# Kernel tuning notes

Measured on AMD Instinct MI355X. Metric: run time of the kernel, lower is better.

## Reference

```python
import jax, jax.numpy as jnp
import numpy as np

NUM_HEADS = 8
DIM_HEAD = 64
GROUPS = 32
EPS = 1e-5


def setup_inputs() -> dict:
    key = jax.random.key(0)
    k1, k2, k3 = jax.random.split(key, 3)
    C = 512
    inner = NUM_HEADS * DIM_HEAD  # 512
    x = jax.random.normal(k1, (8, C, 32, 32), dtype=jnp.float32)
    gamma = jnp.ones((C,), dtype=jnp.float32)
    beta = jnp.zeros((C,), dtype=jnp.float32)
    w_qkv = jax.random.normal(k2, (3 * inner, C), dtype=jnp.float32) * 0.02
    w_out = jax.random.normal(k3, (C, inner), dtype=jnp.float32) * 0.02
    return {"x": x, "gamma": gamma, "beta": beta, "w_qkv": w_qkv, "w_out": w_out}


def group_norm(x, gamma, beta):
    b, c, h, w = x.shape
    xg = x.reshape(b, GROUPS, c // GROUPS, h, w)
    mean = jnp.mean(xg, axis=(2, 3, 4), keepdims=True)
    var = jnp.var(xg, axis=(2, 3, 4), keepdims=True)
    xn = ((xg - mean) * jax.lax.rsqrt(var + EPS)).reshape(b, c, h, w)
    return xn * gamma[None, :, None, None] + beta[None, :, None, None]


def reference(x, gamma, beta, w_qkv, w_out):
    b, c, h, w = x.shape
    H, d = NUM_HEADS, DIM_HEAD
    inner = H * d
    scale = d ** (-0.5)
    residual = x
    xn = group_norm(x, gamma, beta)
    # 1x1 conv (no bias) == channel matmul
    qkv = jnp.einsum('bchw,oc->bohw', xn, w_qkv)  # [b, 3*inner, h, w]
    q, k, v = jnp.split(qkv, 3, axis=1)
    def to_heads(t):
        # b (H d) h w -> b H (h w) d
        return t.reshape(b, H, d, h * w).transpose(0, 1, 3, 2)
    q, k, v = to_heads(q), to_heads(k), to_heads(v)
    attn = jnp.einsum('bhid,bhjd->bhij', q, k) * scale  # [b,H,hw,hw]
    attn = jax.nn.softmax(attn, axis=-1)
    out = jnp.einsum('bhij,bhjd->bhid', attn, v)  # [b,H,hw,d]
    # b H (h w) d -> b (H d) h w
    out = out.transpose(0, 1, 3, 2).reshape(b, inner, h, w)
    out = jnp.einsum('bchw,oc->bohw', out, w_out)
    return out + residual
```

## Files before the change

kernel.cpp:

```cpp
#include <hip/hip_runtime.h>


typedef __attribute__((ext_vector_type(8))) short bf16x8;
typedef __attribute__((ext_vector_type(4))) short bf16x4;
typedef __attribute__((ext_vector_type(4))) float f32x4;

#define NB 8
#define NC 512
#define HW 1024
#define NHEAD 8
#define DHEAD 64
#define GROUPS 32
#define CPG 16
#define QKV_N 1536

#define GLL16(gaddr, ldsaddr)                                                  \
    __builtin_amdgcn_global_load_lds(                                          \
        (const __attribute__((address_space(1))) unsigned*)(gaddr),            \
        (__attribute__((address_space(3))) unsigned*)(ldsaddr), 16, 0, 0)

__device__ alignas(64) short g_xn[(size_t)8192 * 512];
__device__ alignas(64) short g_qkv[(size_t)8192 * 1536];
__device__ alignas(64) short g_vt[(size_t)64 * 64 * 1024];
__device__ alignas(64) short g_attno[(size_t)8192 * 512];
__device__ alignas(64) short g_wqkv[(size_t)1536 * 512];
__device__ alignas(64) short g_wout[(size_t)512 * 512];

__device__ __forceinline__ float b2f(short h) {
    union { unsigned u; float f; } v;
    v.u = ((unsigned)(unsigned short)h) << 16;
    return v.f;
}
__device__ __forceinline__ short f2b(float f) {
    union { float f; unsigned u; } v;
    v.f = f;
    unsigned r = v.u + 0x7fff + ((v.u >> 16) & 1);
    return (short)(r >> 16);
}

__global__ __launch_bounds__(256) void prep_kernel(
    const float* __restrict__ x, const float* __restrict__ gamma,
    const float* __restrict__ beta, const float* __restrict__ wqkv,
    const float* __restrict__ wout) {
    int tid = threadIdx.x;
    if (blockIdx.x >= 256) {
        int wb = blockIdx.x - 256;
        for (int i = wb * 256 + tid; i < 1536 * 512; i += 64 * 256) {
            float v = wqkv[i];
            if (i < 512 * 512) v *= 0.18033688011112042f;
            g_wqkv[i] = f2b(v);
        }
        for (int i = wb * 256 + tid; i < 512 * 512; i += 64 * 256)
            g_wout[i] = f2b(wout[i]);
        return;
    }
    int b = blockIdx.x >> 5, g = blockIdx.x & 31;
    __shared__ alignas(16) short tile[CPG][HW];
    __shared__ float red[2][4];
    __shared__ float sg[CPG], sb[CPG];
    if (tid < CPG) {
        int cg = g * CPG + tid;
        sg[tid] = gamma[cg];
        sb[tid] = beta[cg];
    }
    const float* xb = x + (size_t)b * NC * HW + (size_t)g * CPG * HW;
    float s1 = 0.f, s2 = 0.f;
    #pragma unroll
    for (int it = 0; it < 8; it++) {
        int idx = tid + it * 256;
        f32x4 v0 = *(const f32x4*)(xb + idx * 8);
        f32x4 v1 = *(const f32x4*)(xb + idx * 8 + 4);
        bf16x8 w;
        #pragma unroll
        for (int j = 0; j < 4; j++) {
            s1 += v0[j] + v1[j]; s2 += v0[j] * v0[j] + v1[j] * v1[j];
            w[j] = f2b(v0[j]); w[j + 4] = f2b(v1[j]);
        }
        *(bf16x8*)(&((short*)tile)[idx * 8]) = w;
    }
    #pragma unroll
    for (int off = 32; off; off >>= 1) { s1 += __shfl_xor(s1, off); s2 += __shfl_xor(s2, off); }
    int wid = tid >> 6;
    if ((tid & 63) == 0) { red[0][wid] = s1; red[1][wid] = s2; }
    __syncthreads();
    float t1 = red[0][0] + red[0][1] + red[0][2] + red[0][3];
    float t2 = red[1][0] + red[1][1] + red[1][2] + red[1][3];
    float mean = t1 * (1.f / 16384.f);
    float var  = t2 * (1.f / 16384.f) - mean * mean;
    float inv  = rsqrtf(var + 1e-5f);
    #pragma unroll
    for (int p = 0; p < 4; p++) {
        int s = tid * 4 + p;
        bf16x8 pk0, pk1;
        #pragma unroll
        for (int cc = 0; cc < 8; cc++) {
            pk0[cc] = f2b((b2f(tile[cc][s])     - mean) * inv * sg[cc]     + sb[cc]);
            pk1[cc] = f2b((b2f(tile[cc + 8][s]) - mean) * inv * sg[cc + 8] + sb[cc + 8]);
        }
        size_t dst = ((size_t)(b * HW + s)) * NC + g * CPG;
        *(bf16x8*)(g_xn + dst)     = pk0;
        *(bf16x8*)(g_xn + dst + 8) = pk1;
    }
}

__global__ __launch_bounds__(256) void gemm_qkv() {
    const int K = NC;
    int tid = threadIdx.x, lane = tid & 63, wid = tid >> 6;
    int quad = lane >> 4, l15 = lane & 15;
    int row0 = blockIdx.x * 128;
    int col0 = blockIdx.y * 128;
    __shared__ alignas(16) short sa[128 * 64];
    __shared__ alignas(16) short sbuf[128 * 64];
    int r_lo = lane >> 3;
    int s_log = (lane & 7) ^ r_lo;
    int swz = l15 & 7;
    const short* ga = g_xn   + (size_t)(row0 + wid * 32 + r_lo) * K + s_log * 8;
    const short* gb = g_wqkv + (size_t)(col0 + wid * 32 + r_lo) * K + s_log * 8;
    int mw = (wid >> 1) * 64, nw = (wid & 1) * 64;
    f32x4 acc[4][4] = {};
    for (int k = 0; k < K; k += 64) {
        #pragma unroll
        for (int c = 0; c < 4; c++) {
            GLL16(ga + (size_t)(c * 8) * K + k, &sa[(wid * 32 + c * 8) * 64]);
            GLL16(gb + (size_t)(c * 8) * K + k, &sbuf[(wid * 32 + c * 8) * 64]);
        }
        __syncthreads();
        bf16x8 af0[4], af1[4], bf0[4], bf1[4];
        #pragma unroll
        for (int m = 0; m < 4; m++) {
            int row = mw + m * 16 + l15;
            af0[m] = *(const bf16x8*)&sa[row * 64 + ((quad ^ swz) * 8)];
            af1[m] = *(const bf16x8*)&sa[row * 64 + (((4 + quad) ^ swz) * 8)];
        }
        #pragma unroll
        for (int n = 0; n < 4; n++) {
            int row = nw + n * 16 + l15;
            bf0[n] = *(const bf16x8*)&sbuf[row * 64 + ((quad ^ swz) * 8)];
            bf1[n] = *(const bf16x8*)&sbuf[row * 64 + (((4 + quad) ^ swz) * 8)];
        }
        #pragma unroll
        for (int m = 0; m < 4; m++)
            #pragma unroll
            for (int n = 0; n < 4; n++) {
                acc[m][n] = __builtin_amdgcn_mfma_f32_16x16x32_bf16(af0[m], bf0[n], acc[m][n], 0, 0, 0);
                acc[m][n] = __builtin_amdgcn_mfma_f32_16x16x32_bf16(af1[m], bf1[n], acc[m][n], 0, 0, 0);
            }
        __syncthreads();
    }
    #pragma unroll
    for (int m = 0; m < 4; m++)
        #pragma unroll
        for (int n = 0; n < 4; n++)
            #pragma unroll
            for (int r = 0; r < 4; r++) {
                int row = row0 + mw + m * 16 + quad * 4 + r;
                int col = col0 + nw + n * 16 + l15;
                g_qkv[(size_t)row * QKV_N + col] = f2b(acc[m][n][r]);
            }
}

__global__ __launch_bounds__(256) void transpose_v() {
    int bh = blockIdx.x & 63, st = blockIdx.x >> 6;
    int b = bh >> 3, h = bh & 7;
    int tid = threadIdx.x;
    __shared__ alignas(16) short tile[64][72];
    int s0 = st * 64;
    #pragma unroll
    for (int cc = 0; cc < 2; cc++) {
        int idx = tid + cc * 256;
        int s = idx >> 3, dc = idx & 7;
        *(bf16x8*)&tile[s][dc * 8] =
            *(const bf16x8*)(g_qkv + ((size_t)(b * HW + s0 + s)) * QKV_N + 1024 + h * DHEAD + dc * 8);
    }
    __syncthreads();
    #pragma unroll
    for (int cc = 0; cc < 2; cc++) {
        int idx = tid + cc * 256;
        int d = idx & 63, sc = idx >> 6;
        bf16x8 o;
        #pragma unroll
        for (int j = 0; j < 8; j++) o[j] = tile[sc * 8 + j][d];
        *(bf16x8*)(g_vt + ((size_t)(bh * 64 + d)) * HW + s0 + sc * 8) = o;
    }
}

__global__ __launch_bounds__(256) void attn_kernel() {
    int bh = blockIdx.x & 63, qt = blockIdx.x >> 6;
    int b = bh >> 3, h = bh & 7;
    int tid = threadIdx.x, lane = tid & 63, wid = tid >> 6;
    int quad = lane >> 4, l15 = lane & 15;
    __shared__ alignas(16) short kt[2][64 * 64];
    __shared__ alignas(16) short vt[2][64 * 64];
    __shared__ alignas(16) short pt4[4][16][32][4];
    int qrow0 = qt * 128 + wid * 32;

    const short* qb0 = g_qkv + ((size_t)(b * HW + qrow0 + l15)) * QKV_N + h * DHEAD + quad * 8;
    const short* qb1 = g_qkv + ((size_t)(b * HW + qrow0 + 16 + l15)) * QKV_N + h * DHEAD + quad * 8;
    bf16x8 aq0 = *(const bf16x8*)qb0;
    bf16x8 aq1 = *(const bf16x8*)(qb0 + 32);
    bf16x8 aq2 = *(const bf16x8*)qb1;
    bf16x8 aq3 = *(const bf16x8*)(qb1 + 32);
    f32x4 acc_o[2][4] = {};
    f32x4 acc_l[2] = {};
    bf16x8 vone;
    #pragma unroll
    for (int j = 0; j < 8; j++) vone[j] = (short)0x3f80;

    int r_lo = lane >> 3;
    int s_log = (lane & 7) ^ r_lo;
    int swz = l15 & 7;

    auto stage = [&](int it, int bufi) {
        int t0 = it * 64;
        #pragma unroll
        for (int c = 0; c < 2; c++) {
            int r = wid * 16 + c * 8 + r_lo;
            GLL16(g_qkv + ((size_t)(b * HW + t0 + r)) * QKV_N + 512 + h * DHEAD + s_log * 8,
                  &kt[bufi][(wid * 16 + c * 8) * 64]);
            GLL16(g_vt + ((size_t)(bh * 64 + r)) * HW + t0 + s_log * 8,
                  &vt[bufi][(wid * 16 + c * 8) * 64]);
        }
    };

    stage(0, 0);
    __syncthreads();
    for (int it = 0; it < 16; it++) {
        int cur = it & 1;
        if (it < 15) stage(it + 1, cur ^ 1);
        #pragma unroll
        for (int sub = 0; sub < 4; sub++) {
            int row = sub * 16 + l15;
            bf16x8 k0 = *(const bf16x8*)&kt[cur][row * 64 + ((quad ^ swz) * 8)];
            bf16x8 k1 = *(const bf16x8*)&kt[cur][row * 64 + (((4 + quad) ^ swz) * 8)];
            f32x4 z0 = {}, z1 = {};
            z0 = __builtin_amdgcn_mfma_f32_16x16x32_bf16(k0, aq0, z0, 0, 0, 0);
            z0 = __builtin_amdgcn_mfma_f32_16x16x32_bf16(k1, aq1, z0, 0, 0, 0);
            z1 = __builtin_amdgcn_mfma_f32_16x16x32_bf16(k0, aq2, z1, 0, 0, 0);
            z1 = __builtin_amdgcn_mfma_f32_16x16x32_bf16(k1, aq3, z1, 0, 0, 0);
            #pragma unroll
            for (int g = 0; g < 2; g++) {
                f32x4 z = g ? z1 : z0;
                float e0, e1, e2, e3;
                asm("v_exp_f32 %0, %1" : "=v"(e0) : "v"(z[0]));
                asm("v_exp_f32 %0, %1" : "=v"(e1) : "v"(z[1]));
                asm("v_exp_f32 %0, %1" : "=v"(e2) : "v"(z[2]));
                asm("v_exp_f32 %0, %1" : "=v"(e3) : "v"(z[3]));
                union { unsigned w[2]; bf16x4 s; } pk;
                asm("v_cvt_pk_bf16_f32 %0, %1, %2" : "=v"(pk.w[0]) : "v"(e0), "v"(e1));
                asm("v_cvt_pk_bf16_f32 %0, %1, %2" : "=v"(pk.w[1]) : "v"(e2), "v"(e3));
                *(bf16x4*)&pt4[wid][sub * 4 + quad][g * 16 + l15][0] = pk.s;
            }
        }
        asm volatile("" ::: "memory");
        bf16x8 ap[2][2];
        #pragma unroll
        for (int g = 0; g < 2; g++) {
            union { bf16x4 hh[2]; bf16x8 v; } cc;
            cc.hh[0] = *(const bf16x4*)&pt4[wid][quad * 2][g * 16 + l15][0];
            cc.hh[1] = *(const bf16x4*)&pt4[wid][quad * 2 + 1][g * 16 + l15][0];
            ap[g][0] = cc.v;
            cc.hh[0] = *(const bf16x4*)&pt4[wid][8 + quad * 2][g * 16 + l15][0];
            cc.hh[1] = *(const bf16x4*)&pt4[wid][8 + quad * 2 + 1][g * 16 + l15][0];
            ap[g][1] = cc.v;
        }
        acc_l[0] = __builtin_amdgcn_mfma_f32_16x16x32_bf16(ap[0][0], vone, acc_l[0], 0, 0, 0);
        acc_l[0] = __builtin_amdgcn_mfma_f32_16x16x32_bf16(ap[0][1], vone, acc_l[0], 0, 0, 0);
        acc_l[1] = __builtin_amdgcn_mfma_f32_16x16x32_bf16(ap[1][0], vone, acc_l[1], 0, 0, 0);
        acc_l[1] = __builtin_amdgcn_mfma_f32_16x16x32_bf16(ap[1][1], vone, acc_l[1], 0, 0, 0);
        #pragma unroll
        for (int nd = 0; nd < 4; nd++) {
            int row = nd * 16 + l15;
            bf16x8 bv0 = *(const bf16x8*)&vt[cur][row * 64 + ((quad ^ swz) * 8)];
            bf16x8 bv1 = *(const bf16x8*)&vt[cur][row * 64 + (((4 + quad) ^ swz) * 8)];
            acc_o[0][nd] = __builtin_amdgcn_mfma_f32_16x16x32_bf16(ap[0][0], bv0, acc_o[0][nd], 0, 0, 0);
            acc_o[0][nd] = __builtin_amdgcn_mfma_f32_16x16x32_bf16(ap[0][1], bv1, acc_o[0][nd], 0, 0, 0);
            acc_o[1][nd] = __builtin_amdgcn_mfma_f32_16x16x32_bf16(ap[1][0], bv0, acc_o[1][nd], 0, 0, 0);
            acc_o[1][nd] = __builtin_amdgcn_mfma_f32_16x16x32_bf16(ap[1][1], bv1, acc_o[1][nd], 0, 0, 0);
        }
        __syncthreads();
    }
    #pragma unroll
    for (int g = 0; g < 2; g++) {
        #pragma unroll
        for (int r = 0; r < 4; r++) {
            float invl = 1.f / acc_l[g][r];
            size_t row = (size_t)(b * HW + qrow0 + g * 16 + quad * 4 + r);
            #pragma unroll
            for (int nd = 0; nd < 4; nd++)
                g_attno[row * NC + h * DHEAD + nd * 16 + l15] = f2b(acc_o[g][nd][r] * invl);
        }
    }
}

__global__ __launch_bounds__(256) void gemm_out(
    const float* __restrict__ xres, float* __restrict__ out) {
    const int K = NC;
    int tid = threadIdx.x, lane = tid & 63, wid = tid >> 6;
    int quad = lane >> 4, l15 = lane & 15;
    int row0 = blockIdx.x * 128;
    int col0 = blockIdx.y * 128;
    __shared__ alignas(16) short sa[128 * 32];
    __shared__ alignas(16) short sbuf[128 * 32];
    int srow = wid * 32 + (lane >> 2);
    int scol = (lane & 3) * 8;
    const short* ga = g_wout  + (size_t)(row0 + srow) * K + scol;
    const short* gb = g_attno + (size_t)(col0 + srow) * K + scol;
    short* la = sa   + wid * 1024;
    short* lb = sbuf + wid * 1024;
    int mw = (wid >> 1) * 64, nw = (wid & 1) * 64;
    f32x4 acc[4][4] = {};
    for (int k = 0; k < K; k += 32) {
        GLL16(ga + k, la);
        GLL16(ga + (size_t)16 * K + k, la + 512);
        GLL16(gb + k, lb);
        GLL16(gb + (size_t)16 * K + k, lb + 512);
        __syncthreads();
        bf16x8 af[4], bfv[4];
        #pragma unroll
        for (int m = 0; m < 4; m++) af[m]  = *(const bf16x8*)&sa[(mw + m * 16 + l15) * 32 + quad * 8];
        #pragma unroll
        for (int n = 0; n < 4; n++) bfv[n] = *(const bf16x8*)&sbuf[(nw + n * 16 + l15) * 32 + quad * 8];
        #pragma unroll
        for (int m = 0; m < 4; m++)
            #pragma unroll
            for (int n = 0; n < 4; n++)
                acc[m][n] = __builtin_amdgcn_mfma_f32_16x16x32_bf16(af[m], bfv[n], acc[m][n], 0, 0, 0);
        __syncthreads();
    }
    #pragma unroll
    for (int m = 0; m < 4; m++)
        #pragma unroll
        for (int n = 0; n < 4; n++)
            #pragma unroll
            for (int r = 0; r < 4; r++) {
                int o  = row0 + mw + m * 16 + quad * 4 + r;
                int bs = col0 + nw + n * 16 + l15;
                size_t addr = (size_t)(bs >> 10) * ((size_t)NC * HW) + (size_t)o * HW + (bs & 1023);
                out[addr] = acc[m][n][r] + xres[addr];
            }
}

extern "C" void kernel_launch(void* const* d_in, const int* in_sizes, int n_in,
                              void* d_out, int out_size, void* d_ws, size_t ws_size,
                              hipStream_t stream) {
    const float* x     = (const float*)d_in[0];
    const float* gamma = (const float*)d_in[1];
    const float* beta  = (const float*)d_in[2];
    const float* wqkv  = (const float*)d_in[3];
    const float* wout  = (const float*)d_in[4];
    float* out = (float*)d_out;

    prep_kernel<<<dim3(320), dim3(256), 0, stream>>>(x, gamma, beta, wqkv, wout);
    gemm_qkv<<<dim3(64, 12), dim3(256), 0, stream>>>();
    transpose_v<<<dim3(1024), dim3(256), 0, stream>>>();
    attn_kernel<<<dim3(512), dim3(256), 0, stream>>>();
    gemm_out<<<dim3(4, 64), dim3(256), 0, stream>>>(x, out);
}
```

Baseline: 155.8 us.

## Software-pipeline attention: compute next tile's QK/exp while doing current PV

Restructures the attention main loop so the QK^T MFMA, exp and bf16 pack for tile it+1 are issued in the same iteration as the P·V and row-sum MFMAs for tile it. The probability scratch buffer pt4 is double-buffered, and V fragments are loaded into registers before the barrier so the K/V buffer can be refilled two tiles ahead. A prologue and an epilogue handle the first and last tiles. The aim is to overlap VALU exp work with matrix-core work and cut the per-iteration barrier stalls. The cost is extra LDS, higher register pressure from the held V fragments, and a longer code path.

```diff
diff --git a/kernel.cpp b/kernel.cpp
--- a/kernel.cpp
+++ b/kernel.cpp
@@ -191,7 +191,7 @@
     int quad = lane >> 4, l15 = lane & 15;
     __shared__ alignas(16) short kt[2][64 * 64];
     __shared__ alignas(16) short vt[2][64 * 64];
-    __shared__ alignas(16) short pt4[4][16][32][4];
+    __shared__ alignas(16) short pt4[2][4][16][32][4];
     int qrow0 = qt * 128 + wid * 32;
 
     const short* qb0 = g_qkv + ((size_t)(b * HW + qrow0 + l15)) * QKV_N + h * DHEAD + quad * 8;
@@ -222,16 +222,12 @@
         }
     };
 
-    stage(0, 0);
-    __syncthreads();
-    for (int it = 0; it < 16; it++) {
-        int cur = it & 1;
-        if (it < 15) stage(it + 1, cur ^ 1);
+    auto qk_exppack = [&](int buf) {
         #pragma unroll
         for (int sub = 0; sub < 4; sub++) {
             int row = sub * 16 + l15;
-            bf16x8 k0 = *(const bf16x8*)&kt[cur][row * 64 + ((quad ^ swz) * 8)];
-            bf16x8 k1 = *(const bf16x8*)&kt[cur][row * 64 + (((4 + quad) ^ swz) * 8)];
+            bf16x8 k0 = *(const bf16x8*)&kt[buf][row * 64 + ((quad ^ swz) * 8)];
+            bf16x8 k1 = *(const bf16x8*)&kt[buf][row * 64 + (((4 + quad) ^ swz) * 8)];
             f32x4 z0 = {}, z1 = {};
             z0 = __builtin_amdgcn_mfma_f32_16x16x32_bf16(k0, aq0, z0, 0, 0, 0);
             z0 = __builtin_amdgcn_mfma_f32_16x16x32_bf16(k1, aq1, z0, 0, 0, 0);
@@ -248,36 +244,78 @@
                 union { unsigned w[2]; bf16x4 s; } pk;
                 asm("v_cvt_pk_bf16_f32 %0, %1, %2" : "=v"(pk.w[0]) : "v"(e0), "v"(e1));
                 asm("v_cvt_pk_bf16_f32 %0, %1, %2" : "=v"(pk.w[1]) : "v"(e2), "v"(e3));
-                *(bf16x4*)&pt4[wid][sub * 4 + quad][g * 16 + l15][0] = pk.s;
+                *(bf16x4*)&pt4[buf][wid][sub * 4 + quad][g * 16 + l15][0] = pk.s;
             }
         }
         asm volatile("" ::: "memory");
+    };
+
+    stage(0, 0);
+    __syncthreads();
+    stage(1, 1);
+    qk_exppack(0);
+
+    for (int it = 0; it < 15; it++) {
+        int cur = it & 1, alt = cur ^ 1;
         bf16x8 ap[2][2];
         #pragma unroll
         for (int g = 0; g < 2; g++) {
             union { bf16x4 hh[2]; bf16x8 v; } cc;
-            cc.hh[0] = *(const bf16x4*)&pt4[wid][quad * 2][g * 16 + l15][0];
-            cc.hh[1] = *(const bf16x4*)&pt4[wid][quad * 2 + 1][g * 16 + l15][0];
+            cc.hh[0] = *(const bf16x4*)&pt4[cur][wid][quad * 2][g * 16 + l15][0];
+            cc.hh[1] = *(const bf16x4*)&pt4[cur][wid][quad * 2 + 1][g * 16 + l15][0];
             ap[g][0] = cc.v;
-            cc.hh[0] = *(const bf16x4*)&pt4[wid][8 + quad * 2][g * 16 + l15][0];
-            cc.hh[1] = *(const bf16x4*)&pt4[wid][8 + quad * 2 + 1][g * 16 + l15][0];
+            cc.hh[0] = *(const bf16x4*)&pt4[cur][wid][8 + quad * 2][g * 16 + l15][0];
+            cc.hh[1] = *(const bf16x4*)&pt4[cur][wid][8 + quad * 2 + 1][g * 16 + l15][0];
             ap[g][1] = cc.v;
         }
+        bf16x8 bv[4][2];
+        #pragma unroll
+        for (int nd = 0; nd < 4; nd++) {
+            int row = nd * 16 + l15;
+            bv[nd][0] = *(const bf16x8*)&vt[cur][row * 64 + ((quad ^ swz) * 8)];
+            bv[nd][1] = *(const bf16x8*)&vt[cur][row * 64 + (((4 + quad) ^ swz) * 8)];
+        }
+        __syncthreads();
+        if (it < 14) stage(it + 2, cur);
+        qk_exppack(alt);
         acc_l[0] = __builtin_amdgcn_mfma_f32_16x16x32_bf16(ap[0][0], vone, acc_l[0], 0, 0, 0);
         acc_l[0] = __builtin_amdgcn_mfma_f32_16x16x32_bf16(ap[0][1], vone, acc_l[0], 0, 0, 0);
         acc_l[1] = __builtin_amdgcn_mfma_f32_16x16x32_bf16(ap[1][0], vone, acc_l[1], 0, 0, 0);
         acc_l[1] = __builtin_amdgcn_mfma_f32_16x16x32_bf16(ap[1][1], vone, acc_l[1], 0, 0, 0);
         #pragma unroll
         for (int nd = 0; nd < 4; nd++) {
+            acc_o[0][nd] = __builtin_amdgcn_mfma_f32_16x16x32_bf16(ap[0][0], bv[nd][0], acc_o[0][nd], 0, 0, 0);
+            acc_o[0][nd] = __builtin_amdgcn_mfma_f32_16x16x32_bf16(ap[0][1], bv[nd][1], acc_o[0][nd], 0, 0, 0);
+            acc_o[1][nd] = __builtin_amdgcn_mfma_f32_16x16x32_bf16(ap[1][0], bv[nd][0], acc_o[1][nd], 0, 0, 0);
+            acc_o[1][nd] = __builtin_amdgcn_mfma_f32_16x16x32_bf16(ap[1][1], bv[nd][1], acc_o[1][nd], 0, 0, 0);
+        }
+    }
+    {
+        bf16x8 ap[2][2];
+        #pragma unroll
+        for (int g = 0; g < 2; g++) {
+            union { bf16x4 hh[2]; bf16x8 v; } cc;
+            cc.hh[0] = *(const bf16x4*)&pt4[1][wid][quad * 2][g * 16 + l15][0];
+            cc.hh[1] = *(const bf16x4*)&pt4[1][wid][quad * 2 + 1][g * 16 + l15][0];
+            ap[g][0] = cc.v;
+            cc.hh[0] = *(const bf16x4*)&pt4[1][wid][8 + quad * 2][g * 16 + l15][0];
+            cc.hh[1] = *(const bf16x4*)&pt4[1][wid][8 + quad * 2 + 1][g * 16 + l15][0];
+            ap[g][1] = cc.v;
+        }
+        acc_l[0] = __builtin_amdgcn_mfma_f32_16x16x32_bf16(ap[0][0], vone, acc_l[0], 0, 0, 0);
+        acc_l[0] = __builtin_amdgcn_mfma_f32_16x16x32_bf16(ap[0][1], vone, acc_l[0], 0, 0, 0);
+        acc_l[1] = __builtin_amdgcn_mfma_f32_16x16x32_bf16(ap[1][0], vone, acc_l[1], 0, 0, 0);
+        acc_l[1] = __builtin_amdgcn_mfma_f32_16x16x32_bf16(ap[1][1], vone, acc_l[1], 0, 0, 0);
+        #pragma unroll
+        for (int nd = 0; nd < 4; nd++) {
             int row = nd * 16 + l15;
-            bf16x8 bv0 = *(const bf16x8*)&vt[cur][row * 64 + ((quad ^ swz) * 8)];
-            bf16x8 bv1 = *(const bf16x8*)&vt[cur][row * 64 + (((4 + quad) ^ swz) * 8)];
+            bf16x8 bv0 = *(const bf16x8*)&vt[1][row * 64 + ((quad ^ swz) * 8)];
+            bf16x8 bv1 = *(const bf16x8*)&vt[1][row * 64 + (((4 + quad) ^ swz) * 8)];
             acc_o[0][nd] = __builtin_amdgcn_mfma_f32_16x16x32_bf16(ap[0][0], bv0, acc_o[0][nd], 0, 0, 0);
             acc_o[0][nd] = __builtin_amdgcn_mfma_f32_16x16x32_bf16(ap[0][1], bv1, acc_o[0][nd], 0, 0, 0);
             acc_o[1][nd] = __builtin_amdgcn_mfma_f32_16x16x32_bf16(ap[1][0], bv0, acc_o[1][nd], 0, 0, 0);
             acc_o[1][nd] = __builtin_amdgcn_mfma_f32_16x16x32_bf16(ap[1][1], bv1, acc_o[1][nd], 0, 0, 0);
         }
-        __syncthreads();
     }
     #pragma unroll
     for (int g = 0; g < 2; g++) {
```

New measurement: 152.4 us. 2.2% less time.

## Load K and V directly from global memory instead of LDS double buffering

Applied to the files above, without the earlier changes.

The attention kernel drops its double-buffered LDS staging of K and V tiles (global_load_lds with swizzle) and the per-iteration barrier. Each wave now reads its K and V fragments straight from global memory, relying on L1/L2 caching across the four waves that share them. This removes the LDS traffic and block-wide synchronisation, but it quadruples global/cache requests and loses the prefetch overlap of the next tile.

```diff
diff --git a/kernel.cpp b/kernel.cpp
--- a/kernel.cpp
+++ b/kernel.cpp
@@ -189,8 +189,6 @@
     int b = bh >> 3, h = bh & 7;
     int tid = threadIdx.x, lane = tid & 63, wid = tid >> 6;
     int quad = lane >> 4, l15 = lane & 15;
-    __shared__ alignas(16) short kt[2][64 * 64];
-    __shared__ alignas(16) short vt[2][64 * 64];
     __shared__ alignas(16) short pt4[4][16][32][4];
     int qrow0 = qt * 128 + wid * 32;
 
@@ -206,32 +204,16 @@
     #pragma unroll
     for (int j = 0; j < 8; j++) vone[j] = (short)0x3f80;
 
-    int r_lo = lane >> 3;
-    int s_log = (lane & 7) ^ r_lo;
-    int swz = l15 & 7;
-
-    auto stage = [&](int it, int bufi) {
+    const short* kbase = g_qkv + (size_t)(b * HW) * QKV_N + 512 + h * DHEAD;
+    const short* vbase = g_vt + (size_t)(bh * 64) * HW;
+
+    for (int it = 0; it < 16; it++) {
         int t0 = it * 64;
         #pragma unroll
-        for (int c = 0; c < 2; c++) {
-            int r = wid * 16 + c * 8 + r_lo;
-            GLL16(g_qkv + ((size_t)(b * HW + t0 + r)) * QKV_N + 512 + h * DHEAD + s_log * 8,
-                  &kt[bufi][(wid * 16 + c * 8) * 64]);
-            GLL16(g_vt + ((size_t)(bh * 64 + r)) * HW + t0 + s_log * 8,
-                  &vt[bufi][(wid * 16 + c * 8) * 64]);
-        }
-    };
-
-    stage(0, 0);
-    __syncthreads();
-    for (int it = 0; it < 16; it++) {
-        int cur = it & 1;
-        if (it < 15) stage(it + 1, cur ^ 1);
-        #pragma unroll
         for (int sub = 0; sub < 4; sub++) {
-            int row = sub * 16 + l15;
-            bf16x8 k0 = *(const bf16x8*)&kt[cur][row * 64 + ((quad ^ swz) * 8)];
-            bf16x8 k1 = *(const bf16x8*)&kt[cur][row * 64 + (((4 + quad) ^ swz) * 8)];
+            size_t trow = (size_t)(t0 + sub * 16 + l15) * QKV_N;
+            bf16x8 k0 = *(const bf16x8*)(kbase + trow + quad * 8);
+            bf16x8 k1 = *(const bf16x8*)(kbase + trow + (4 + quad) * 8);
             f32x4 z0 = {}, z1 = {};
             z0 = __builtin_amdgcn_mfma_f32_16x16x32_bf16(k0, aq0, z0, 0, 0, 0);
             z0 = __builtin_amdgcn_mfma_f32_16x16x32_bf16(k1, aq1, z0, 0, 0, 0);
@@ -269,15 +251,14 @@
         acc_l[1] = __builtin_amdgcn_mfma_f32_16x16x32_bf16(ap[1][1], vone, acc_l[1], 0, 0, 0);
         #pragma unroll
         for (int nd = 0; nd < 4; nd++) {
-            int row = nd * 16 + l15;
-            bf16x8 bv0 = *(const bf16x8*)&vt[cur][row * 64 + ((quad ^ swz) * 8)];
-            bf16x8 bv1 = *(const bf16x8*)&vt[cur][row * 64 + (((4 + quad) ^ swz) * 8)];
+            size_t drow = (size_t)(nd * 16 + l15) * HW;
+            bf16x8 bv0 = *(const bf16x8*)(vbase + drow + t0 + quad * 8);
+            bf16x8 bv1 = *(const bf16x8*)(vbase + drow + t0 + (4 + quad) * 8);
             acc_o[0][nd] = __builtin_amdgcn_mfma_f32_16x16x32_bf16(ap[0][0], bv0, acc_o[0][nd], 0, 0, 0);
             acc_o[0][nd] = __builtin_amdgcn_mfma_f32_16x16x32_bf16(ap[0][1], bv1, acc_o[0][nd], 0, 0, 0);
             acc_o[1][nd] = __builtin_amdgcn_mfma_f32_16x16x32_bf16(ap[1][0], bv0, acc_o[1][nd], 0, 0, 0);
             acc_o[1][nd] = __builtin_amdgcn_mfma_f32_16x16x32_bf16(ap[1][1], bv1, acc_o[1][nd], 0, 0, 0);
         }
-        __syncthreads();
     }
     #pragma unroll
     for (int g = 0; g < 2; g++) {
```

Result: slower. 183.7 us (+17.9%).
